# Kernel tuning notes

Measured on AMD Instinct MI355X. Metric: run time of the kernel, lower is better.

## Reference

```python
import jax, jax.numpy as jnp
import numpy as np

DIM = 32
HID = 128          # edge-MLP hidden width
N = 8192           # total nodes
E = 131072         # total edges
B = 64             # number of graphs
NUM_MP = 3
S2S_STEPS = 3


def setup_inputs() -> dict:
    key = jax.random.key(0)
    ks = jax.random.split(key, 24)
    g = lambda k, shape, s=0.05: jax.random.normal(k, shape, dtype=jnp.float32) * s

    inp = {
        "x": jax.random.normal(ks[0], (N, 1), dtype=jnp.float32),
        "edge_attr": jax.random.uniform(ks[1], (E, 2), dtype=jnp.float32),
        # params
        "lin0_w": g(ks[2], (1, DIM)), "lin0_b": g(ks[3], (DIM,)),
        "enn_w1": g(ks[4], (2, HID)), "enn_b1": g(ks[5], (HID,)),
        "enn_w2": g(ks[6], (HID, DIM * DIM)), "enn_b2": g(ks[7], (DIM * DIM,)),
        "root_w": g(ks[8], (DIM, DIM)), "conv_b": g(ks[9], (DIM,)),
        # GRU (gates ordered r,z,n as in torch)
        "gru_wih": g(ks[10], (DIM, 3 * DIM)), "gru_whh": g(ks[11], (DIM, 3 * DIM)),
        "gru_bih": g(ks[12], (3 * DIM,)), "gru_bhh": g(ks[13], (3 * DIM,)),
        # Set2Set LSTM: input 2*DIM, hidden DIM (gates ordered i,f,g,o as in torch)
        "s2s_wih": g(ks[14], (2 * DIM, 4 * DIM)), "s2s_whh": g(ks[15], (DIM, 4 * DIM)),
        "s2s_bih": g(ks[16], (4 * DIM,)), "s2s_bhh": g(ks[17], (4 * DIM,)),
        "lin1_w": g(ks[18], (2 * DIM, DIM)), "lin1_b": g(ks[19], (DIM,)),
        "lin2_w": g(ks[20], (DIM, 1)), "lin2_b": g(ks[21], (1,)),
        # int args
        "edge_index": jax.random.randint(ks[22], (2, E), 0, N, dtype=jnp.int32),
        "batch": jnp.sort(jax.random.randint(ks[23], (N,), 0, B, dtype=jnp.int32)),
    }
    return inp


def _forward(x, edge_attr, lin0_w, lin0_b, enn_w1, enn_b1, enn_w2, enn_b2,
             root_w, conv_b, gru_wih, gru_whh, gru_bih, gru_bhh,
             s2s_wih, s2s_whh, s2s_bih, s2s_bhh, lin1_w, lin1_b, lin2_w, lin2_b,
             edge_index, batch):
    src, dst = edge_index[0], edge_index[1]

    out = jax.nn.relu(x @ lin0_w + lin0_b)          # [N, DIM]
    h = out                                          # GRU hidden state

    # edge-conditioned weights (constant across MP layers -> hoisted)
    ew = jax.nn.relu(edge_attr @ enn_w1 + enn_b1) @ enn_w2 + enn_b2
    W = ew.reshape(E, DIM, DIM)                      # [E, in, out]

    deg = jnp.maximum(jax.ops.segment_sum(jnp.ones((E,), jnp.float32), dst,
                                          num_segments=N), 1.0)[:, None]

    for _ in range(NUM_MP):
        # NNConv: gather -> per-edge small matmul -> scatter-mean, + root + bias
        msg = jnp.einsum('ed,edo->eo', out[src], W)  # [E, DIM]
        agg = jax.ops.segment_sum(msg, dst, num_segments=N) / deg
        m = jax.nn.relu(agg + out @ root_w + conv_b)
        # GRU cell (single step)
        gi = m @ gru_wih + gru_bih
        gh = h @ gru_whh + gru_bhh
        ir, iz, in_ = jnp.split(gi, 3, axis=-1)
        hr, hz, hn = jnp.split(gh, 3, axis=-1)
        r = jax.nn.sigmoid(ir + hr)
        z = jax.nn.sigmoid(iz + hz)
        n = jnp.tanh(in_ + r * hn)
        h = (1.0 - z) * n + z * h
        out = h

    # Set2Set pooling
    qh = jnp.zeros((B, DIM), jnp.float32)
    qc = jnp.zeros((B, DIM), jnp.float32)
    q_star = jnp.zeros((B, 2 * DIM), jnp.float32)
    for _ in range(S2S_STEPS):
        gates = q_star @ s2s_wih + s2s_bih + qh @ s2s_whh + s2s_bhh
        i_, f_, g_, o_ = jnp.split(gates, 4, axis=-1)
        qc = jax.nn.sigmoid(f_) * qc + jax.nn.sigmoid(i_) * jnp.tanh(g_)
        qh = jax.nn.sigmoid(o_) * jnp.tanh(qc)       # [B, DIM]
        e = jnp.sum(out * qh[batch], axis=-1)        # [N] attention logits
        emax = jax.ops.segment_max(e, batch, num_segments=B)
        a = jnp.exp(e - emax[batch])
        a = a / jax.ops.segment_sum(a, batch, num_segments=B)[batch]
        r_read = jax.ops.segment_sum(a[:, None] * out, batch, num_segments=B)
        q_star = jnp.concatenate([qh, r_read], axis=-1)  # [B, 2*DIM]

    y = jax.nn.relu(q_star @ lin1_w + lin1_b) @ lin2_w + lin2_b
    return y.reshape(-1)                              # [B]


def reference(x, edge_attr, lin0_w, lin0_b, enn_w1, enn_b1, enn_w2, enn_b2,
              root_w, conv_b, gru_wih, gru_whh, gru_bih, gru_bhh,
              s2s_wih, s2s_whh, s2s_bih, s2s_bhh, lin1_w, lin1_b, lin2_w, lin2_b,
              edge_index, batch):
    return _forward(x, edge_attr, lin0_w, lin0_b, enn_w1, enn_b1, enn_w2, enn_b2,
                    root_w, conv_b, gru_wih, gru_whh, gru_bih, gru_bhh,
                    s2s_wih, s2s_whh, s2s_bih, s2s_bhh, lin1_w, lin1_b, lin2_w,
                    lin2_b, edge_index, batch)
```

## Files before the change

### kernel.cpp

```cpp
#include <hip/hip_runtime.h>

#define N_NODES 8192
#define N_EDGES 131072
#define NGRAPH  64
#define DIM     32
#define HID     128
#define KHALF   64
#define G_NODES 4
#define SROW    36
#define HROW    68
#define OROW    36
#define CEDGE   64
#define S2S_CAP 384

__device__ __forceinline__ float sigmoidf_(float x) { return 1.0f / (1.0f + expf(-x)); }

__global__ void prep1_kernel(const float* __restrict__ x, const float* __restrict__ w,
                             const float* __restrict__ b, float* __restrict__ out,
                             const int* __restrict__ dst, int* __restrict__ counts) {
  const int bb = blockIdx.x;
  if (bb < 1024) {
    int idx = bb * 256 + threadIdx.x;
    int n = idx >> 5, d = idx & 31;
    out[idx] = fmaxf(fmaf(x[n], w[d], b[d]), 0.0f);
  } else {
    int e = (bb - 1024) * 256 + threadIdx.x;
    atomicAdd(&counts[dst[e]], 1);
  }
}

__global__ void scan_kernel(const int* __restrict__ counts,
                            int* __restrict__ offsets,
                            float* __restrict__ deg_inv) {
  __shared__ int sm[1024];
  int t = threadIdx.x;
  int base = t * 8;
  int loc[8];
  int s = 0;
#pragma unroll
  for (int i = 0; i < 8; ++i) { loc[i] = s; s += counts[base + i]; }
  sm[t] = s;
  __syncthreads();
  for (int off = 1; off < 1024; off <<= 1) {
    int v = (t >= off) ? sm[t - off] : 0;
    __syncthreads();
    sm[t] += v;
    __syncthreads();
  }
  int excl = (t > 0) ? sm[t - 1] : 0;
#pragma unroll
  for (int i = 0; i < 8; ++i) {
    offsets[base + i] = excl + loc[i];
    int c = counts[base + i];
    deg_inv[base + i] = 1.0f / (float)(c > 0 ? c : 1);
  }
  if (t == 1023) offsets[N_NODES] = sm[1023];
}

__global__ void prep2_kernel(const int* __restrict__ ei, const float* __restrict__ ea,
                             const int* __restrict__ offsets, int* __restrict__ cursor,
                             int* __restrict__ csr_src, float2* __restrict__ csr_ea,
                             const int* __restrict__ batch, int* __restrict__ gstart) {
  const int bb = blockIdx.x;
  if (bb < 512) {
    int e = bb * 256 + threadIdx.x;
    int d = ei[N_EDGES + e];
    int pos = atomicAdd(&cursor[d], 1);
    int slot = offsets[d] + pos;
    csr_src[slot] = ei[e];
    csr_ea[slot] = make_float2(ea[2 * e], ea[2 * e + 1]);
  } else {
    int n = (bb - 512) * 256 + threadIdx.x;
    int b = batch[n];
    if (n == 0) {
      for (int g = 0; g <= b; ++g) gstart[g] = 0;
    } else {
      int bp = batch[n - 1];
      for (int g = bp + 1; g <= b; ++g) gstart[g] = n;
    }
    if (n == N_NODES - 1) {
      for (int g = b + 1; g <= NGRAPH; ++g) gstart[g] = N_NODES;
    }
  }
}

__global__ __launch_bounds__(256, 4) void mp_kernel(
    const float* __restrict__ out_cur, float* __restrict__ out_nxt,
    const int* __restrict__ offsets, const float* __restrict__ deg_inv,
    const int* __restrict__ csr_src, const float2* __restrict__ csr_ea,
    const float* __restrict__ w1, const float* __restrict__ b1,
    const float* __restrict__ w2, const float* __restrict__ b2,
    const float* __restrict__ root_w, const float* __restrict__ conv_b,
    const float* __restrict__ gwih, const float* __restrict__ gwhh,
    const float* __restrict__ gbih, const float* __restrict__ gbhh) {
  __shared__ float smem[G_NODES * KHALF * SROW];
  __shared__ float w1s[3 * HID];
  __shared__ float ebuf[G_NODES * DIM];
  __shared__ float mbuf[G_NODES * DIM];
  __shared__ float obuf[G_NODES * DIM];
  __shared__ int offs[G_NODES + 1];
  float* hidb = smem;
  float* osrcb = smem + CEDGE * HROW;
  float* S = smem;
  float* red = smem;

  const int t = threadIdx.x;
  const int node0 = blockIdx.x * G_NODES;

  if (t <= G_NODES) offs[t] = offsets[node0 + t];
  if (t < HID) {
    w1s[t] = w1[t];
    w1s[HID + t] = w1[HID + t];
    w1s[2 * HID + t] = b1[t];
  }

  const int kg = t >> 4, dg = t & 15;
  const int k0 = kg * 4, d0 = dg * 2;
  const int ec = t >> 2, sub = t & 3;
  const int ks = t >> 4;
  const int dvh = (t >> 3) & 1;
  const int og = t & 7;

  float a4[G_NODES][4];
#pragma unroll
  for (int g = 0; g < G_NODES; ++g)
#pragma unroll
    for (int r = 0; r < 4; ++r) a4[g][r] = 0.0f;
  float oacc[G_NODES] = {0.0f, 0.0f, 0.0f, 0.0f};
  __syncthreads();

  const int ebase = offs[0], eend = offs[G_NODES];

  for (int half = 0; half < 2; ++half) {
    float acc[G_NODES][4][2];
#pragma unroll
    for (int g = 0; g < G_NODES; ++g)
#pragma unroll
      for (int i = 0; i < 4; ++i) { acc[g][i][0] = 0.0f; acc[g][i][1] = 0.0f; }

    for (int c0 = ebase; c0 < eend; c0 += CEDGE) {
      const int cnt = min(CEDGE, eend - c0);
      if (ec < cnt) {
        const int slot = c0 + ec;
        const float2 eav = csr_ea[slot];
        const int sidx = csr_src[slot];
#pragma unroll
        for (int q = 0; q < 4; ++q) {
          const int kl = sub * 16 + q * 4;
          const int kgl = half * KHALF + kl;
          const float4 wx = *(const float4*)(w1s + kgl);
          const float4 wy = *(const float4*)(w1s + HID + kgl);
          const float4 bv = *(const float4*)(w1s + 2 * HID + kgl);
          float4 hv;
          hv.x = fmaxf(fmaf(eav.y, wy.x, fmaf(eav.x, wx.x, bv.x)), 0.0f);
          hv.y = fmaxf(fmaf(eav.y, wy.y, fmaf(eav.x, wx.y, bv.y)), 0.0f);
          hv.z = fmaxf(fmaf(eav.y, wy.z, fmaf(eav.x, wx.z, bv.z)), 0.0f);
          hv.w = fmaxf(fmaf(eav.y, wy.w, fmaf(eav.x, wx.w, bv.w)), 0.0f);
          *(float4*)(hidb + ec * HROW + kl) = hv;
        }
        *(float4*)(osrcb + ec * OROW + sub * 8) =
            *(const float4*)(out_cur + sidx * DIM + sub * 8);
        *(float4*)(osrcb + ec * OROW + sub * 8 + 4) =
            *(const float4*)(out_cur + sidx * DIM + sub * 8 + 4);
      }
      __syncthreads();
#pragma unroll
      for (int g = 0; g < G_NODES; ++g) {
        const int es = max(offs[g], c0) - c0;
        const int ee = min(offs[g + 1], c0 + cnt) - c0;
        for (int e = es; e < ee; ++e) {
          const float4 hv = *(const float4*)(hidb + e * HROW + k0);
          const float2 ov = *(const float2*)(osrcb + e * OROW + d0);
          acc[g][0][0] = fmaf(hv.x, ov.x, acc[g][0][0]);
          acc[g][0][1] = fmaf(hv.x, ov.y, acc[g][0][1]);
          acc[g][1][0] = fmaf(hv.y, ov.x, acc[g][1][0]);
          acc[g][1][1] = fmaf(hv.y, ov.y, acc[g][1][1]);
          acc[g][2][0] = fmaf(hv.z, ov.x, acc[g][2][0]);
          acc[g][2][1] = fmaf(hv.z, ov.y, acc[g][2][1]);
          acc[g][3][0] = fmaf(hv.w, ov.x, acc[g][3][0]);
          acc[g][3][1] = fmaf(hv.w, ov.y, acc[g][3][1]);
          if (half == 0 && t < DIM) oacc[g] += osrcb[e * OROW + t];
        }
      }
      __syncthreads();
    }

    {
      const int dd = (d0 + (kg & 3) * 8) & 31;
#pragma unroll
      for (int g = 0; g < G_NODES; ++g) {
        float* Sg = S + g * KHALF * SROW;
#pragma unroll
        for (int i = 0; i < 4; ++i)
          *(float2*)(Sg + (k0 + i) * SROW + dd) =
              make_float2(acc[g][i][0], acc[g][i][1]);
      }
    }
    __syncthreads();

    {
      const int shift = (ks & 3) * 8;
#pragma unroll
      for (int i = 0; i < 4; ++i) {
        const int kl = ks * 4 + i;
        const float* w2k = w2 + (size_t)(half * KHALF + kl) * (DIM * DIM);
#pragma unroll
        for (int q = 0; q < 4; ++q) {
          const int dbase = dvh * 16 + q * 4;
          const int dq = (dbase + shift) & 31;
          float4 sv[G_NODES];
#pragma unroll
          for (int g = 0; g < G_NODES; ++g)
            sv[g] = *(const float4*)(S + (g * KHALF + kl) * SROW + dq);
#pragma unroll
          for (int r = 0; r < 4; ++r) {
            const float4 wv = *(const float4*)(w2k + (dbase + r) * DIM + og * 4);
#pragma unroll
            for (int g = 0; g < G_NODES; ++g) {
              const float s = ((const float*)&sv[g])[r];
              a4[g][0] = fmaf(s, wv.x, a4[g][0]);
              a4[g][1] = fmaf(s, wv.y, a4[g][1]);
              a4[g][2] = fmaf(s, wv.z, a4[g][2]);
              a4[g][3] = fmaf(s, wv.w, a4[g][3]);
            }
          }
        }
      }
    }
    __syncthreads();
  }

#pragma unroll
  for (int g = 0; g < G_NODES; ++g)
#pragma unroll
    for (int r = 0; r < 4; ++r) red[(g * 4 + r) * 257 + t] = a4[g][r];
  if (t < DIM) {
#pragma unroll
    for (int g = 0; g < G_NODES; ++g) obuf[g * DIM + t] = oacc[g];
  }
  if (t < G_NODES * DIM) ebuf[t] = out_cur[node0 * DIM + t];
  __syncthreads();

  if (t < G_NODES * DIM) {
    const int g = t >> 5, o = t & 31;
    const int node = node0 + g;
    const float* rp = red + (g * 4 + (o & 3)) * 257 + (o >> 2);
    float sum = 0.0f;
#pragma unroll
    for (int j = 0; j < 32; ++j) sum += rp[j * 8];
    float ob2 = 0.0f;
#pragma unroll
    for (int d = 0; d < DIM; ++d) ob2 = fmaf(obuf[g * DIM + d], b2[d * DIM + o], ob2);
    const float agg = (sum + ob2) * deg_inv[node];
    float rt = conv_b[o];
#pragma unroll
    for (int d = 0; d < DIM; ++d) rt = fmaf(ebuf[g * DIM + d], root_w[d * DIM + o], rt);
    mbuf[t] = fmaxf(agg + rt, 0.0f);
  }
  __syncthreads();
  if (t < G_NODES * DIM) {
    const int g = t >> 5, o = t & 31;
    const int node = node0 + g;
    float gi[3], gh[3];
#pragma unroll
    for (int jj = 0; jj < 3; ++jj) {
      float si = gbih[jj * DIM + o], sh = gbhh[jj * DIM + o];
#pragma unroll
      for (int d = 0; d < DIM; ++d) {
        si = fmaf(mbuf[g * DIM + d], gwih[d * 3 * DIM + jj * DIM + o], si);
        sh = fmaf(ebuf[g * DIM + d], gwhh[d * 3 * DIM + jj * DIM + o], sh);
      }
      gi[jj] = si;
      gh[jj] = sh;
    }
    const float r = sigmoidf_(gi[0] + gh[0]);
    const float z = sigmoidf_(gi[1] + gh[1]);
    const float nn = tanhf(fmaf(r, gh[2], gi[2]));
    out_nxt[node * DIM + o] = (1.0f - z) * nn + z * ebuf[t];
  }
}

__global__ __launch_bounds__(256) void s2s_kernel(
    const float* __restrict__ outf, const int* __restrict__ gstart,
    const float* __restrict__ wih, const float* __restrict__ whh,
    const float* __restrict__ bih, const float* __restrict__ bhh,
    const float* __restrict__ l1w, const float* __restrict__ l1b,
    const float* __restrict__ l2w, const float* __restrict__ l2b,
    float* __restrict__ y) {
  __shared__ float rows[S2S_CAP * DIM];
  __shared__ float qh[DIM], qc[DIM], qstar[2 * DIM], gates[4 * DIM];
  __shared__ float wsum[4], wmax[4], wr[4][DIM];
  const int b = blockIdx.x, t = threadIdx.x;
  const int gs = gstart[b], ge = gstart[b + 1];
  const int cnt = ge - gs;
  const int w = t >> 6, lane = t & 63;
  const bool use_lds = (cnt <= S2S_CAP);
  if (use_lds) {
    for (int j = t * 4; j < cnt * DIM; j += 1024)
      *(float4*)(rows + j) = *(const float4*)(outf + (size_t)gs * DIM + j);
  }
  const float* R = use_lds ? (const float*)rows : outf + (size_t)gs * DIM;
  if (t < DIM) { qh[t] = 0.0f; qc[t] = 0.0f; }
  if (t < 2 * DIM) qstar[t] = 0.0f;
  __syncthreads();
  for (int step = 0; step < 3; ++step) {
    if (t < 4 * DIM) {
      float gv = bih[t] + bhh[t];
      for (int i = 0; i < 2 * DIM; ++i) gv = fmaf(qstar[i], wih[i * 4 * DIM + t], gv);
      for (int i = 0; i < DIM; ++i) gv = fmaf(qh[i], whh[i * 4 * DIM + t], gv);
      gates[t] = gv;
    }
    __syncthreads();
    if (t < DIM) {
      const float ig = sigmoidf_(gates[t]);
      const float fg = sigmoidf_(gates[DIM + t]);
      const float gg = tanhf(gates[2 * DIM + t]);
      const float og = sigmoidf_(gates[3 * DIM + t]);
      const float c = fmaf(fg, qc[t], ig * gg);
      qc[t] = c;
      qh[t] = og * tanhf(c);
    }
    __syncthreads();
    float lmax = -INFINITY;
    for (int n = t; n < cnt; n += 256) {
      const float* orow = R + n * DIM;
      float e = 0.0f;
#pragma unroll
      for (int d = 0; d < DIM; ++d) e = fmaf(orow[d], qh[d], e);
      lmax = fmaxf(lmax, e);
    }
#pragma unroll
    for (int off = 32; off > 0; off >>= 1) lmax = fmaxf(lmax, __shfl_xor(lmax, off));
    if (lane == 0) wmax[w] = lmax;
    __syncthreads();
    const float gmax = fmaxf(fmaxf(wmax[0], wmax[1]), fmaxf(wmax[2], wmax[3]));
    float rl[DIM];
#pragma unroll
    for (int d = 0; d < DIM; ++d) rl[d] = 0.0f;
    float lsum = 0.0f;
    for (int n = t; n < cnt; n += 256) {
      const float* orow = R + n * DIM;
      float e = 0.0f;
#pragma unroll
      for (int d = 0; d < DIM; ++d) e = fmaf(orow[d], qh[d], e);
      const float a = expf(e - gmax);
      lsum += a;
#pragma unroll
      for (int d = 0; d < DIM; ++d) rl[d] = fmaf(a, orow[d], rl[d]);
    }
#pragma unroll
    for (int off = 32; off > 0; off >>= 1) {
      lsum += __shfl_xor(lsum, off);
#pragma unroll
      for (int d = 0; d < DIM; ++d) rl[d] += __shfl_xor(rl[d], off);
    }
    __syncthreads();
    if (lane == 0) {
      wsum[w] = lsum;
#pragma unroll
      for (int d = 0; d < DIM; ++d) wr[w][d] = rl[d];
    }
    __syncthreads();
    if (t < DIM) {
      const float stot = wsum[0] + wsum[1] + wsum[2] + wsum[3];
      const float rv = wr[0][t] + wr[1][t] + wr[2][t] + wr[3][t];
      qstar[t] = qh[t];
      qstar[DIM + t] = (stot > 0.0f) ? rv / stot : 0.0f;
    }
    __syncthreads();
  }
  if (t < DIM) {
    float u = l1b[t];
    for (int i = 0; i < 2 * DIM; ++i) u = fmaf(qstar[i], l1w[i * DIM + t], u);
    u = fmaxf(u, 0.0f);
    float v = u * l2w[t];
#pragma unroll
    for (int off = 16; off > 0; off >>= 1) v += __shfl_xor(v, off);
    if (t == 0) y[b] = v + l2b[0];
  }
}

extern "C" void kernel_launch(void* const* d_in, const int* in_sizes, int n_in,
                              void* d_out, int out_size, void* d_ws, size_t ws_size,
                              hipStream_t stream) {
  const float* x        = (const float*)d_in[0];
  const float* ea       = (const float*)d_in[1];
  const float* lin0_w   = (const float*)d_in[2];
  const float* lin0_b   = (const float*)d_in[3];
  const float* enn_w1   = (const float*)d_in[4];
  const float* enn_b1   = (const float*)d_in[5];
  const float* enn_w2   = (const float*)d_in[6];
  const float* enn_b2   = (const float*)d_in[7];
  const float* root_w   = (const float*)d_in[8];
  const float* conv_b   = (const float*)d_in[9];
  const float* gru_wih  = (const float*)d_in[10];
  const float* gru_whh  = (const float*)d_in[11];
  const float* gru_bih  = (const float*)d_in[12];
  const float* gru_bhh  = (const float*)d_in[13];
  const float* s2s_wih  = (const float*)d_in[14];
  const float* s2s_whh  = (const float*)d_in[15];
  const float* s2s_bih  = (const float*)d_in[16];
  const float* s2s_bhh  = (const float*)d_in[17];
  const float* lin1_w   = (const float*)d_in[18];
  const float* lin1_b   = (const float*)d_in[19];
  const float* lin2_w   = (const float*)d_in[20];
  const float* lin2_b   = (const float*)d_in[21];
  const int*   ei       = (const int*)d_in[22];
  const int*   batch    = (const int*)d_in[23];
  float* y = (float*)d_out;

  char* p = (char*)d_ws;
  auto alloc = [&](size_t bytes) -> void* {
    void* r = (void*)p;
    p += (bytes + 255) & ~(size_t)255;
    return r;
  };
  float*  out_a   = (float*)alloc(N_NODES * DIM * 4);
  float*  out_b   = (float*)alloc(N_NODES * DIM * 4);
  int*    counts  = (int*)alloc(N_NODES * 4);
  int*    cursor  = (int*)alloc(N_NODES * 4);
  int*    offsets = (int*)alloc((N_NODES + 1) * 4);
  int*    csr_src = (int*)alloc(N_EDGES * 4);
  float2* csr_ea  = (float2*)alloc(N_EDGES * 8);
  float*  deg_inv = (float*)alloc(N_NODES * 4);
  int*    gstart  = (int*)alloc((NGRAPH + 1) * 4);
  (void)ws_size; (void)n_in; (void)in_sizes; (void)out_size;

  hipMemsetAsync(counts, 0, (size_t)2 * N_NODES * 4, stream);

  prep1_kernel<<<1024 + 512, 256, 0, stream>>>(x, lin0_w, lin0_b, out_a,
                                               ei + N_EDGES, counts);
  scan_kernel<<<1, 1024, 0, stream>>>(counts, offsets, deg_inv);
  prep2_kernel<<<512 + 32, 256, 0, stream>>>(ei, ea, offsets, cursor, csr_src,
                                             csr_ea, batch, gstart);

  const int ngroups = N_NODES / G_NODES;
  const float* cur = out_a;
  float* nxt = out_b;
  for (int layer = 0; layer < 3; ++layer) {
    mp_kernel<<<ngroups, 256, 0, stream>>>(
        cur, nxt, offsets, deg_inv, csr_src, csr_ea, enn_w1, enn_b1, enn_w2,
        enn_b2, root_w, conv_b, gru_wih, gru_whh, gru_bih, gru_bhh);
    const float* tmp = cur; cur = nxt; nxt = (float*)tmp;
  }

  s2s_kernel<<<NGRAPH, 256, 0, stream>>>(cur, gstart, s2s_wih, s2s_whh, s2s_bih,
                                         s2s_bhh, lin1_w, lin1_b, lin2_w, lin2_b, y);
}
```

Measured before the change: 435.0 us.

## Process full 128-wide hidden dimension in one pass instead of two halves

The message-passing kernel used to split the 128-wide edge-MLP hidden dimension into two halves, walking the edge list and recomputing the hidden activations and gathering source features twice. It now handles all 128 hidden units in one edge pass, with each thread holding 4x4 accumulators per node, and stores the full S tile in dynamic LDS (about 73 KB) before one w2 contraction. This removes the duplicated edge gathers, the extra passes and the barriers between them. The cost is much higher LDS and register use per block, with launch bounds lowered to 2 blocks, so occupancy drops.

Measured after the change: 1.014 ms. 2.33x slower.

```diff
diff --git a/kernel.cpp b/kernel.cpp
--- a/kernel.cpp
+++ b/kernel.cpp
@@ -5,13 +5,13 @@
 #define NGRAPH  64
 #define DIM     32
 #define HID     128
-#define KHALF   64
 #define G_NODES 4
 #define SROW    36
-#define HROW    68
+#define HROW    132
 #define OROW    36
 #define CEDGE   64
 #define S2S_CAP 384
+#define DYN_LDS (G_NODES * HID * SROW * 4)
 
 __device__ __forceinline__ float sigmoidf_(float x) { return 1.0f / (1.0f + expf(-x)); }
 
@@ -84,7 +84,7 @@
   }
 }
 
-__global__ __launch_bounds__(256, 4) void mp_kernel(
+__global__ __launch_bounds__(256, 2) void mp_kernel(
     const float* __restrict__ out_cur, float* __restrict__ out_nxt,
     const int* __restrict__ offsets, const float* __restrict__ deg_inv,
     const int* __restrict__ csr_src, const float2* __restrict__ csr_ea,
@@ -93,7 +93,7 @@
     const float* __restrict__ root_w, const float* __restrict__ conv_b,
     const float* __restrict__ gwih, const float* __restrict__ gwhh,
     const float* __restrict__ gbih, const float* __restrict__ gbhh) {
-  __shared__ float smem[G_NODES * KHALF * SROW];
+  extern __shared__ float smem[];
   __shared__ float w1s[3 * HID];
   __shared__ float ebuf[G_NODES * DIM];
   __shared__ float mbuf[G_NODES * DIM];
@@ -114,131 +114,128 @@
     w1s[2 * HID + t] = b1[t];
   }
 
-  const int kg = t >> 4, dg = t & 15;
-  const int k0 = kg * 4, d0 = dg * 2;
+  const int kg = t >> 3, dg = t & 7;
+  const int k0 = kg * 4, d0 = dg * 4;
   const int ec = t >> 2, sub = t & 3;
-  const int ks = t >> 4;
-  const int dvh = (t >> 3) & 1;
-  const int og = t & 7;
+
+  float acc[G_NODES][4][4];
+#pragma unroll
+  for (int g = 0; g < G_NODES; ++g)
+#pragma unroll
+    for (int i = 0; i < 4; ++i)
+#pragma unroll
+      for (int j = 0; j < 4; ++j) acc[g][i][j] = 0.0f;
+  float oacc[G_NODES] = {0.0f, 0.0f, 0.0f, 0.0f};
+  __syncthreads();
+
+  const int ebase = offs[0], eend = offs[G_NODES];
+  for (int c0 = ebase; c0 < eend; c0 += CEDGE) {
+    const int cnt = min(CEDGE, eend - c0);
+    if (ec < cnt) {
+      const int slot = c0 + ec;
+      const float2 eav = csr_ea[slot];
+      const int sidx = csr_src[slot];
+#pragma unroll
+      for (int q = 0; q < 8; ++q) {
+        const int k4 = sub * 32 + q * 4;
+        const float4 wx = *(const float4*)(w1s + k4);
+        const float4 wy = *(const float4*)(w1s + HID + k4);
+        const float4 bv = *(const float4*)(w1s + 2 * HID + k4);
+        float4 hv;
+        hv.x = fmaxf(fmaf(eav.y, wy.x, fmaf(eav.x, wx.x, bv.x)), 0.0f);
+        hv.y = fmaxf(fmaf(eav.y, wy.y, fmaf(eav.x, wx.y, bv.y)), 0.0f);
+        hv.z = fmaxf(fmaf(eav.y, wy.z, fmaf(eav.x, wx.z, bv.z)), 0.0f);
+        hv.w = fmaxf(fmaf(eav.y, wy.w, fmaf(eav.x, wx.w, bv.w)), 0.0f);
+        *(float4*)(hidb + ec * HROW + k4) = hv;
+      }
+      *(float4*)(osrcb + ec * OROW + sub * 8) =
+          *(const float4*)(out_cur + sidx * DIM + sub * 8);
+      *(float4*)(osrcb + ec * OROW + sub * 8 + 4) =
+          *(const float4*)(out_cur + sidx * DIM + sub * 8 + 4);
+    }
+    __syncthreads();
+#pragma unroll
+    for (int g = 0; g < G_NODES; ++g) {
+      const int es = max(offs[g], c0) - c0;
+      const int ee = min(offs[g + 1], c0 + cnt) - c0;
+      for (int e = es; e < ee; ++e) {
+        const float4 hv = *(const float4*)(hidb + e * HROW + k0);
+        const float4 ov = *(const float4*)(osrcb + e * OROW + d0);
+        acc[g][0][0] = fmaf(hv.x, ov.x, acc[g][0][0]);
+        acc[g][0][1] = fmaf(hv.x, ov.y, acc[g][0][1]);
+        acc[g][0][2] = fmaf(hv.x, ov.z, acc[g][0][2]);
+        acc[g][0][3] = fmaf(hv.x, ov.w, acc[g][0][3]);
+        acc[g][1][0] = fmaf(hv.y, ov.x, acc[g][1][0]);
+        acc[g][1][1] = fmaf(hv.y, ov.y, acc[g][1][1]);
+        acc[g][1][2] = fmaf(hv.y, ov.z, acc[g][1][2]);
+        acc[g][1][3] = fmaf(hv.y, ov.w, acc[g][1][3]);
+        acc[g][2][0] = fmaf(hv.z, ov.x, acc[g][2][0]);
+        acc[g][2][1] = fmaf(hv.z, ov.y, acc[g][2][1]);
+        acc[g][2][2] = fmaf(hv.z, ov.z, acc[g][2][2]);
+        acc[g][2][3] = fmaf(hv.z, ov.w, acc[g][2][3]);
+        acc[g][3][0] = fmaf(hv.w, ov.x, acc[g][3][0]);
+        acc[g][3][1] = fmaf(hv.w, ov.y, acc[g][3][1]);
+        acc[g][3][2] = fmaf(hv.w, ov.z, acc[g][3][2]);
+        acc[g][3][3] = fmaf(hv.w, ov.w, acc[g][3][3]);
+        if (t < DIM) oacc[g] += osrcb[e * OROW + t];
+      }
+    }
+    __syncthreads();
+  }
+
+#pragma unroll
+  for (int g = 0; g < G_NODES; ++g) {
+#pragma unroll
+    for (int i = 0; i < 4; ++i)
+      *(float4*)(S + (g * HID + k0 + i) * SROW + d0) =
+          make_float4(acc[g][i][0], acc[g][i][1], acc[g][i][2], acc[g][i][3]);
+  }
+  if (t < DIM) {
+#pragma unroll
+    for (int g = 0; g < G_NODES; ++g) obuf[g * DIM + t] = oacc[g];
+  }
+  if (t < G_NODES * DIM) ebuf[t] = out_cur[node0 * DIM + t];
+  __syncthreads();
 
   float a4[G_NODES][4];
 #pragma unroll
   for (int g = 0; g < G_NODES; ++g)
 #pragma unroll
     for (int r = 0; r < 4; ++r) a4[g][r] = 0.0f;
-  float oacc[G_NODES] = {0.0f, 0.0f, 0.0f, 0.0f};
-  __syncthreads();
-
-  const int ebase = offs[0], eend = offs[G_NODES];
-
-  for (int half = 0; half < 2; ++half) {
-    float acc[G_NODES][4][2];
-#pragma unroll
-    for (int g = 0; g < G_NODES; ++g)
-#pragma unroll
-      for (int i = 0; i < 4; ++i) { acc[g][i][0] = 0.0f; acc[g][i][1] = 0.0f; }
-
-    for (int c0 = ebase; c0 < eend; c0 += CEDGE) {
-      const int cnt = min(CEDGE, eend - c0);
-      if (ec < cnt) {
-        const int slot = c0 + ec;
-        const float2 eav = csr_ea[slot];
-        const int sidx = csr_src[slot];
-#pragma unroll
-        for (int q = 0; q < 4; ++q) {
-          const int kl = sub * 16 + q * 4;
-          const int kgl = half * KHALF + kl;
-          const float4 wx = *(const float4*)(w1s + kgl);
-          const float4 wy = *(const float4*)(w1s + HID + kgl);
-          const float4 bv = *(const float4*)(w1s + 2 * HID + kgl);
-          float4 hv;
-          hv.x = fmaxf(fmaf(eav.y, wy.x, fmaf(eav.x, wx.x, bv.x)), 0.0f);
-          hv.y = fmaxf(fmaf(eav.y, wy.y, fmaf(eav.x, wx.y, bv.y)), 0.0f);
-          hv.z = fmaxf(fmaf(eav.y, wy.z, fmaf(eav.x, wx.z, bv.z)), 0.0f);
-          hv.w = fmaxf(fmaf(eav.y, wy.w, fmaf(eav.x, wx.w, bv.w)), 0.0f);
-          *(float4*)(hidb + ec * HROW + kl) = hv;
-        }
-        *(float4*)(osrcb + ec * OROW + sub * 8) =
-            *(const float4*)(out_cur + sidx * DIM + sub * 8);
-        *(float4*)(osrcb + ec * OROW + sub * 8 + 4) =
-            *(const float4*)(out_cur + sidx * DIM + sub * 8 + 4);
-      }
-      __syncthreads();
-#pragma unroll
-      for (int g = 0; g < G_NODES; ++g) {
-        const int es = max(offs[g], c0) - c0;
-        const int ee = min(offs[g + 1], c0 + cnt) - c0;
-        for (int e = es; e < ee; ++e) {
-          const float4 hv = *(const float4*)(hidb + e * HROW + k0);
-          const float2 ov = *(const float2*)(osrcb + e * OROW + d0);
-          acc[g][0][0] = fmaf(hv.x, ov.x, acc[g][0][0]);
-          acc[g][0][1] = fmaf(hv.x, ov.y, acc[g][0][1]);
-          acc[g][1][0] = fmaf(hv.y, ov.x, acc[g][1][0]);
-          acc[g][1][1] = fmaf(hv.y, ov.y, acc[g][1][1]);
-          acc[g][2][0] = fmaf(hv.z, ov.x, acc[g][2][0]);
-          acc[g][2][1] = fmaf(hv.z, ov.y, acc[g][2][1]);
-          acc[g][3][0] = fmaf(hv.w, ov.x, acc[g][3][0]);
-          acc[g][3][1] = fmaf(hv.w, ov.y, acc[g][3][1]);
-          if (half == 0 && t < DIM) oacc[g] += osrcb[e * OROW + t];
-        }
-      }
-      __syncthreads();
-    }
-
-    {
-      const int dd = (d0 + (kg & 3) * 8) & 31;
-#pragma unroll
-      for (int g = 0; g < G_NODES; ++g) {
-        float* Sg = S + g * KHALF * SROW;
-#pragma unroll
-        for (int i = 0; i < 4; ++i)
-          *(float2*)(Sg + (k0 + i) * SROW + dd) =
-              make_float2(acc[g][i][0], acc[g][i][1]);
-      }
-    }
-    __syncthreads();
-
-    {
-      const int shift = (ks & 3) * 8;
-#pragma unroll
-      for (int i = 0; i < 4; ++i) {
-        const int kl = ks * 4 + i;
-        const float* w2k = w2 + (size_t)(half * KHALF + kl) * (DIM * DIM);
-#pragma unroll
-        for (int q = 0; q < 4; ++q) {
-          const int dbase = dvh * 16 + q * 4;
-          const int dq = (dbase + shift) & 31;
-          float4 sv[G_NODES];
-#pragma unroll
-          for (int g = 0; g < G_NODES; ++g)
-            sv[g] = *(const float4*)(S + (g * KHALF + kl) * SROW + dq);
-#pragma unroll
-          for (int r = 0; r < 4; ++r) {
-            const float4 wv = *(const float4*)(w2k + (dbase + r) * DIM + og * 4);
-#pragma unroll
-            for (int g = 0; g < G_NODES; ++g) {
-              const float s = ((const float*)&sv[g])[r];
-              a4[g][0] = fmaf(s, wv.x, a4[g][0]);
-              a4[g][1] = fmaf(s, wv.y, a4[g][1]);
-              a4[g][2] = fmaf(s, wv.z, a4[g][2]);
-              a4[g][3] = fmaf(s, wv.w, a4[g][3]);
-            }
+  {
+    const int ks = t >> 3;
+    const int og = t & 7;
+#pragma unroll
+    for (int i = 0; i < 4; ++i) {
+      const int kl = ks * 4 + i;
+      const float* w2k = w2 + (size_t)kl * (DIM * DIM);
+#pragma unroll
+      for (int q = 0; q < 8; ++q) {
+        const int dq = ((q + ks) & 7) * 4;
+        float4 sv[G_NODES];
+#pragma unroll
+        for (int g = 0; g < G_NODES; ++g)
+          sv[g] = *(const float4*)(S + (g * HID + kl) * SROW + dq);
+#pragma unroll
+        for (int r = 0; r < 4; ++r) {
+          const float4 wv = *(const float4*)(w2k + (dq + r) * DIM + og * 4);
+#pragma unroll
+          for (int g = 0; g < G_NODES; ++g) {
+            const float s = ((const float*)&sv[g])[r];
+            a4[g][0] = fmaf(s, wv.x, a4[g][0]);
+            a4[g][1] = fmaf(s, wv.y, a4[g][1]);
+            a4[g][2] = fmaf(s, wv.z, a4[g][2]);
+            a4[g][3] = fmaf(s, wv.w, a4[g][3]);
           }
         }
       }
     }
-    __syncthreads();
-  }
-
+  }
+  __syncthreads();
 #pragma unroll
   for (int g = 0; g < G_NODES; ++g)
 #pragma unroll
     for (int r = 0; r < 4; ++r) red[(g * 4 + r) * 257 + t] = a4[g][r];
-  if (t < DIM) {
-#pragma unroll
-    for (int g = 0; g < G_NODES; ++g) obuf[g * DIM + t] = oacc[g];
-  }
-  if (t < G_NODES * DIM) ebuf[t] = out_cur[node0 * DIM + t];
   __syncthreads();
 
   if (t < G_NODES * DIM) {
@@ -409,6 +406,11 @@
   const int*   batch    = (const int*)d_in[23];
   float* y = (float*)d_out;
 
+  static int lds_set = 0;
+  (void)lds_set;
+  hipFuncSetAttribute((const void*)mp_kernel,
+                      hipFuncAttributeMaxDynamicSharedMemorySize, DYN_LDS);
+
   char* p = (char*)d_ws;
   auto alloc = [&](size_t bytes) -> void* {
     void* r = (void*)p;
@@ -438,7 +440,7 @@
   const float* cur = out_a;
   float* nxt = out_b;
   for (int layer = 0; layer < 3; ++layer) {
-    mp_kernel<<<ngroups, 256, 0, stream>>>(
+    mp_kernel<<<ngroups, 256, DYN_LDS, stream>>>(
         cur, nxt, offsets, deg_inv, csr_src, csr_ea, enn_w1, enn_b1, enn_w2,
         enn_b2, root_w, conv_b, gru_wih, gru_whh, gru_bih, gru_bhh);
     const float* tmp = cur; cur = nxt; nxt = (float*)tmp;
```

## Restructure message-passing kernel: 8 nodes per block, per-wave edge loops, K in four passes

Applied to the files above, without the earlier changes.

The message-passing kernel now handles 8 nodes per block instead of 4. Each wave walks the edges of two nodes directly from global memory, prefetching the next edge's source features into registers, instead of staging 64-edge chunks of hidden activations and source rows in LDS behind block barriers. The hidden dimension is split into four passes of 32, and each pass's W2 contraction now serves 8 nodes, doubling reuse of every W2 load. The cost is more registers (a 64-entry accumulator per thread), load imbalance across waves when node degrees differ, and half as many blocks.

Result: slower. 1.650 ms (+279.4%).

```diff
diff --git a/kernel.cpp b/kernel.cpp
--- a/kernel.cpp
+++ b/kernel.cpp
@@ -5,12 +5,10 @@
 #define NGRAPH  64
 #define DIM     32
 #define HID     128
-#define KHALF   64
-#define G_NODES 4
+#define G_NODES 8
+#define P_K     32
 #define SROW    36
-#define HROW    68
-#define OROW    36
-#define CEDGE   64
+#define RPAD    65
 #define S2S_CAP 384
 
 __device__ __forceinline__ float sigmoidf_(float x) { return 1.0f / (1.0f + expf(-x)); }
@@ -93,135 +91,129 @@
     const float* __restrict__ root_w, const float* __restrict__ conv_b,
     const float* __restrict__ gwih, const float* __restrict__ gwhh,
     const float* __restrict__ gbih, const float* __restrict__ gbhh) {
-  __shared__ float smem[G_NODES * KHALF * SROW];
-  __shared__ float w1s[3 * HID];
+  __shared__ float S[G_NODES * P_K * SROW];
   __shared__ float ebuf[G_NODES * DIM];
-  __shared__ float mbuf[G_NODES * DIM];
+  __shared__ float mbuf[128];
   __shared__ float obuf[G_NODES * DIM];
   __shared__ int offs[G_NODES + 1];
-  float* hidb = smem;
-  float* osrcb = smem + CEDGE * HROW;
-  float* S = smem;
-  float* red = smem;
+  float* red = S;
 
   const int t = threadIdx.x;
   const int node0 = blockIdx.x * G_NODES;
+  const int w = t >> 6, lane = t & 63;
+  const int kg = lane >> 2, dg = lane & 3;
+  const int ks = t >> 4, dq = (t >> 2) & 3, oq = t & 3;
 
   if (t <= G_NODES) offs[t] = offsets[node0 + t];
-  if (t < HID) {
-    w1s[t] = w1[t];
-    w1s[HID + t] = w1[HID + t];
-    w1s[2 * HID + t] = b1[t];
-  }
-
-  const int kg = t >> 4, dg = t & 15;
-  const int k0 = kg * 4, d0 = dg * 2;
-  const int ec = t >> 2, sub = t & 3;
-  const int ks = t >> 4;
-  const int dvh = (t >> 3) & 1;
-  const int og = t & 7;
-
-  float a4[G_NODES][4];
+
+  float a4[G_NODES][8];
 #pragma unroll
   for (int g = 0; g < G_NODES; ++g)
 #pragma unroll
-    for (int r = 0; r < 4; ++r) a4[g][r] = 0.0f;
-  float oacc[G_NODES] = {0.0f, 0.0f, 0.0f, 0.0f};
+    for (int o = 0; o < 8; ++o) a4[g][o] = 0.0f;
   __syncthreads();
 
-  const int ebase = offs[0], eend = offs[G_NODES];
-
-  for (int half = 0; half < 2; ++half) {
-    float acc[G_NODES][4][2];
-#pragma unroll
-    for (int g = 0; g < G_NODES; ++g)
-#pragma unroll
-      for (int i = 0; i < 4; ++i) { acc[g][i][0] = 0.0f; acc[g][i][1] = 0.0f; }
-
-    for (int c0 = ebase; c0 < eend; c0 += CEDGE) {
-      const int cnt = min(CEDGE, eend - c0);
-      if (ec < cnt) {
-        const int slot = c0 + ec;
-        const float2 eav = csr_ea[slot];
-        const int sidx = csr_src[slot];
-#pragma unroll
-        for (int q = 0; q < 4; ++q) {
-          const int kl = sub * 16 + q * 4;
-          const int kgl = half * KHALF + kl;
-          const float4 wx = *(const float4*)(w1s + kgl);
-          const float4 wy = *(const float4*)(w1s + HID + kgl);
-          const float4 bv = *(const float4*)(w1s + 2 * HID + kgl);
-          float4 hv;
-          hv.x = fmaxf(fmaf(eav.y, wy.x, fmaf(eav.x, wx.x, bv.x)), 0.0f);
-          hv.y = fmaxf(fmaf(eav.y, wy.y, fmaf(eav.x, wx.y, bv.y)), 0.0f);
-          hv.z = fmaxf(fmaf(eav.y, wy.z, fmaf(eav.x, wx.z, bv.z)), 0.0f);
-          hv.w = fmaxf(fmaf(eav.y, wy.w, fmaf(eav.x, wx.w, bv.w)), 0.0f);
-          *(float4*)(hidb + ec * HROW + kl) = hv;
+  for (int pass = 0; pass < 4; ++pass) {
+    const int klg0 = pass * P_K + kg * 2;
+    const float2 w1x = *(const float2*)(w1 + klg0);
+    const float2 w1y = *(const float2*)(w1 + HID + klg0);
+    const float2 b1v = *(const float2*)(b1 + klg0);
+#pragma unroll
+    for (int s = 0; s < 2; ++s) {
+      const int g = w * 2 + s;
+      const int eb = offs[g], ee = offs[g + 1];
+      float acc0[8], acc1[8], oacc[8];
+#pragma unroll
+      for (int j = 0; j < 8; ++j) { acc0[j] = 0.0f; acc1[j] = 0.0f; oacc[j] = 0.0f; }
+      float2 ea_n = make_float2(0.0f, 0.0f);
+      float4 ovn0 = make_float4(0, 0, 0, 0), ovn1 = make_float4(0, 0, 0, 0);
+      if (eb < ee) {
+        const int sn = csr_src[eb];
+        ea_n = csr_ea[eb];
+        ovn0 = *(const float4*)(out_cur + sn * DIM + dg * 8);
+        ovn1 = *(const float4*)(out_cur + sn * DIM + dg * 8 + 4);
+      }
+      for (int e = eb; e < ee; ++e) {
+        const float2 eav = ea_n;
+        const float4 ov0 = ovn0, ov1 = ovn1;
+        if (e + 1 < ee) {
+          const int sn = csr_src[e + 1];
+          ea_n = csr_ea[e + 1];
+          ovn0 = *(const float4*)(out_cur + sn * DIM + dg * 8);
+          ovn1 = *(const float4*)(out_cur + sn * DIM + dg * 8 + 4);
         }
-        *(float4*)(osrcb + ec * OROW + sub * 8) =
-            *(const float4*)(out_cur + sidx * DIM + sub * 8);
-        *(float4*)(osrcb + ec * OROW + sub * 8 + 4) =
-            *(const float4*)(out_cur + sidx * DIM + sub * 8 + 4);
-      }
-      __syncthreads();
-#pragma unroll
-      for (int g = 0; g < G_NODES; ++g) {
-        const int es = max(offs[g], c0) - c0;
-        const int ee = min(offs[g + 1], c0 + cnt) - c0;
-        for (int e = es; e < ee; ++e) {
-          const float4 hv = *(const float4*)(hidb + e * HROW + k0);
-          const float2 ov = *(const float2*)(osrcb + e * OROW + d0);
-          acc[g][0][0] = fmaf(hv.x, ov.x, acc[g][0][0]);
-          acc[g][0][1] = fmaf(hv.x, ov.y, acc[g][0][1]);
-          acc[g][1][0] = fmaf(hv.y, ov.x, acc[g][1][0]);
-          acc[g][1][1] = fmaf(hv.y, ov.y, acc[g][1][1]);
-          acc[g][2][0] = fmaf(hv.z, ov.x, acc[g][2][0]);
-          acc[g][2][1] = fmaf(hv.z, ov.y, acc[g][2][1]);
-          acc[g][3][0] = fmaf(hv.w, ov.x, acc[g][3][0]);
-          acc[g][3][1] = fmaf(hv.w, ov.y, acc[g][3][1]);
-          if (half == 0 && t < DIM) oacc[g] += osrcb[e * OROW + t];
+        const float h0 =
+            fmaxf(fmaf(eav.y, w1y.x, fmaf(eav.x, w1x.x, b1v.x)), 0.0f);
+        const float h1 =
+            fmaxf(fmaf(eav.y, w1y.y, fmaf(eav.x, w1x.y, b1v.y)), 0.0f);
+        acc0[0] = fmaf(h0, ov0.x, acc0[0]);
+        acc0[1] = fmaf(h0, ov0.y, acc0[1]);
+        acc0[2] = fmaf(h0, ov0.z, acc0[2]);
+        acc0[3] = fmaf(h0, ov0.w, acc0[3]);
+        acc0[4] = fmaf(h0, ov1.x, acc0[4]);
+        acc0[5] = fmaf(h0, ov1.y, acc0[5]);
+        acc0[6] = fmaf(h0, ov1.z, acc0[6]);
+        acc0[7] = fmaf(h0, ov1.w, acc0[7]);
+        acc1[0] = fmaf(h1, ov0.x, acc1[0]);
+        acc1[1] = fmaf(h1, ov0.y, acc1[1]);
+        acc1[2] = fmaf(h1, ov0.z, acc1[2]);
+        acc1[3] = fmaf(h1, ov0.w, acc1[3]);
+        acc1[4] = fmaf(h1, ov1.x, acc1[4]);
+        acc1[5] = fmaf(h1, ov1.y, acc1[5]);
+        acc1[6] = fmaf(h1, ov1.z, acc1[6]);
+        acc1[7] = fmaf(h1, ov1.w, acc1[7]);
+        if (pass == 0) {
+          oacc[0] += ov0.x; oacc[1] += ov0.y; oacc[2] += ov0.z; oacc[3] += ov0.w;
+          oacc[4] += ov1.x; oacc[5] += ov1.y; oacc[6] += ov1.z; oacc[7] += ov1.w;
         }
       }
-      __syncthreads();
-    }
+      const int rot = (kg & 7) * 4;
+      const int p0 = (dg * 8 + rot) & 31;
+      const int p1 = (dg * 8 + 4 + rot) & 31;
+      float* Sg = S + (g * P_K + kg * 2) * SROW;
+      *(float4*)(Sg + p0) = make_float4(acc0[0], acc0[1], acc0[2], acc0[3]);
+      *(float4*)(Sg + p1) = make_float4(acc0[4], acc0[5], acc0[6], acc0[7]);
+      *(float4*)(Sg + SROW + p0) = make_float4(acc1[0], acc1[1], acc1[2], acc1[3]);
+      *(float4*)(Sg + SROW + p1) = make_float4(acc1[4], acc1[5], acc1[6], acc1[7]);
+      if (pass == 0 && kg == 0) {
+        *(float4*)(obuf + g * DIM + dg * 8) =
+            make_float4(oacc[0], oacc[1], oacc[2], oacc[3]);
+        *(float4*)(obuf + g * DIM + dg * 8 + 4) =
+            make_float4(oacc[4], oacc[5], oacc[6], oacc[7]);
+      }
+    }
+    __syncthreads();
 
     {
-      const int dd = (d0 + (kg & 3) * 8) & 31;
-#pragma unroll
-      for (int g = 0; g < G_NODES; ++g) {
-        float* Sg = S + g * KHALF * SROW;
-#pragma unroll
-        for (int i = 0; i < 4; ++i)
-          *(float2*)(Sg + (k0 + i) * SROW + dd) =
-              make_float2(acc[g][i][0], acc[g][i][1]);
-      }
-    }
-    __syncthreads();
-
-    {
-      const int shift = (ks & 3) * 8;
-#pragma unroll
-      for (int i = 0; i < 4; ++i) {
-        const int kl = ks * 4 + i;
-        const float* w2k = w2 + (size_t)(half * KHALF + kl) * (DIM * DIM);
-#pragma unroll
-        for (int q = 0; q < 4; ++q) {
-          const int dbase = dvh * 16 + q * 4;
-          const int dq = (dbase + shift) & 31;
+      const int rot = (ks & 7) * 4;
+#pragma unroll
+      for (int i = 0; i < 2; ++i) {
+        const int kl = ks * 2 + i;
+        const float* w2k = w2 + (size_t)(pass * P_K + kl) * (DIM * DIM);
+#pragma unroll
+        for (int dd = 0; dd < 2; ++dd) {
+          const int dbase = dq * 8 + dd * 4;
+          const int pos = (dbase + rot) & 31;
           float4 sv[G_NODES];
 #pragma unroll
           for (int g = 0; g < G_NODES; ++g)
-            sv[g] = *(const float4*)(S + (g * KHALF + kl) * SROW + dq);
+            sv[g] = *(const float4*)(S + (g * P_K + kl) * SROW + pos);
 #pragma unroll
           for (int r = 0; r < 4; ++r) {
-            const float4 wv = *(const float4*)(w2k + (dbase + r) * DIM + og * 4);
+            const float* w2d = w2k + (dbase + r) * DIM + oq * 8;
+            const float4 wv0 = *(const float4*)(w2d);
+            const float4 wv1 = *(const float4*)(w2d + 4);
 #pragma unroll
             for (int g = 0; g < G_NODES; ++g) {
-              const float s = ((const float*)&sv[g])[r];
-              a4[g][0] = fmaf(s, wv.x, a4[g][0]);
-              a4[g][1] = fmaf(s, wv.y, a4[g][1]);
-              a4[g][2] = fmaf(s, wv.z, a4[g][2]);
-              a4[g][3] = fmaf(s, wv.w, a4[g][3]);
+              const float sg = ((const float*)&sv[g])[r];
+              a4[g][0] = fmaf(sg, wv0.x, a4[g][0]);
+              a4[g][1] = fmaf(sg, wv0.y, a4[g][1]);
+              a4[g][2] = fmaf(sg, wv0.z, a4[g][2]);
+              a4[g][3] = fmaf(sg, wv0.w, a4[g][3]);
+              a4[g][4] = fmaf(sg, wv1.x, a4[g][4]);
+              a4[g][5] = fmaf(sg, wv1.y, a4[g][5]);
+              a4[g][6] = fmaf(sg, wv1.z, a4[g][6]);
+              a4[g][7] = fmaf(sg, wv1.w, a4[g][7]);
             }
           }
         }
@@ -230,53 +222,57 @@
     __syncthreads();
   }
 
-#pragma unroll
-  for (int g = 0; g < G_NODES; ++g)
-#pragma unroll
-    for (int r = 0; r < 4; ++r) red[(g * 4 + r) * 257 + t] = a4[g][r];
-  if (t < DIM) {
-#pragma unroll
-    for (int g = 0; g < G_NODES; ++g) obuf[g * DIM + t] = oacc[g];
-  }
-  if (t < G_NODES * DIM) ebuf[t] = out_cur[node0 * DIM + t];
-  __syncthreads();
-
-  if (t < G_NODES * DIM) {
-    const int g = t >> 5, o = t & 31;
-    const int node = node0 + g;
-    const float* rp = red + (g * 4 + (o & 3)) * 257 + (o >> 2);
-    float sum = 0.0f;
-#pragma unroll
-    for (int j = 0; j < 32; ++j) sum += rp[j * 8];
-    float ob2 = 0.0f;
-#pragma unroll
-    for (int d = 0; d < DIM; ++d) ob2 = fmaf(obuf[g * DIM + d], b2[d * DIM + o], ob2);
-    const float agg = (sum + ob2) * deg_inv[node];
-    float rt = conv_b[o];
-#pragma unroll
-    for (int d = 0; d < DIM; ++d) rt = fmaf(ebuf[g * DIM + d], root_w[d * DIM + o], rt);
-    mbuf[t] = fmaxf(agg + rt, 0.0f);
-  }
-  __syncthreads();
-  if (t < G_NODES * DIM) {
-    const int g = t >> 5, o = t & 31;
-    const int node = node0 + g;
-    float gi[3], gh[3];
-#pragma unroll
-    for (int jj = 0; jj < 3; ++jj) {
-      float si = gbih[jj * DIM + o], sh = gbhh[jj * DIM + o];
-#pragma unroll
-      for (int d = 0; d < DIM; ++d) {
-        si = fmaf(mbuf[g * DIM + d], gwih[d * 3 * DIM + jj * DIM + o], si);
-        sh = fmaf(ebuf[g * DIM + d], gwhh[d * 3 * DIM + jj * DIM + o], sh);
+  ebuf[t] = out_cur[node0 * DIM + t];
+
+  for (int gb = 0; gb < 2; ++gb) {
+    __syncthreads();
+    const int contrib = ks * 4 + dq;
+#pragma unroll
+    for (int g2 = 0; g2 < 4; ++g2)
+#pragma unroll
+      for (int oo = 0; oo < 8; ++oo)
+        red[(g2 * 32 + oq * 8 + oo) * RPAD + contrib] = a4[gb * 4 + g2][oo];
+    __syncthreads();
+    if (t < 128) {
+      const int g2 = t >> 5, o = t & 31;
+      const int g = gb * 4 + g2;
+      const int node = node0 + g;
+      const float* rp = red + (g2 * 32 + o) * RPAD;
+      float sum = 0.0f;
+#pragma unroll
+      for (int j = 0; j < 64; ++j) sum += rp[j];
+      float ob2 = 0.0f;
+#pragma unroll
+      for (int d = 0; d < DIM; ++d) ob2 = fmaf(obuf[g * DIM + d], b2[d * DIM + o], ob2);
+      const float agg = (sum + ob2) * deg_inv[node];
+      float rt = conv_b[o];
+#pragma unroll
+      for (int d = 0; d < DIM; ++d)
+        rt = fmaf(ebuf[g * DIM + d], root_w[d * DIM + o], rt);
+      mbuf[t] = fmaxf(agg + rt, 0.0f);
+    }
+    __syncthreads();
+    if (t < 128) {
+      const int g2 = t >> 5, o = t & 31;
+      const int g = gb * 4 + g2;
+      const int node = node0 + g;
+      float gi[3], gh[3];
+#pragma unroll
+      for (int jj = 0; jj < 3; ++jj) {
+        float si = gbih[jj * DIM + o], sh = gbhh[jj * DIM + o];
+#pragma unroll
+        for (int d = 0; d < DIM; ++d) {
+          si = fmaf(mbuf[g2 * DIM + d], gwih[d * 3 * DIM + jj * DIM + o], si);
+          sh = fmaf(ebuf[g * DIM + d], gwhh[d * 3 * DIM + jj * DIM + o], sh);
+        }
+        gi[jj] = si;
+        gh[jj] = sh;
       }
-      gi[jj] = si;
-      gh[jj] = sh;
-    }
-    const float r = sigmoidf_(gi[0] + gh[0]);
-    const float z = sigmoidf_(gi[1] + gh[1]);
-    const float nn = tanhf(fmaf(r, gh[2], gi[2]));
-    out_nxt[node * DIM + o] = (1.0f - z) * nn + z * ebuf[t];
+      const float r = sigmoidf_(gi[0] + gh[0]);
+      const float z = sigmoidf_(gi[1] + gh[1]);
+      const float nn = tanhf(fmaf(r, gh[2], gi[2]));
+      out_nxt[node * DIM + o] = (1.0f - z) * nn + z * ebuf[g * DIM + o];
+    }
   }
 }
 
@@ -434,11 +430,11 @@
   prep2_kernel<<<512 + 32, 256, 0, stream>>>(ei, ea, offsets, cursor, csr_src,
                                              csr_ea, batch, gstart);
 
-  const int ngroups = N_NODES / G_NODES;
+  const int nblocks = N_NODES / G_NODES;
   const float* cur = out_a;
   float* nxt = out_b;
   for (int layer = 0; layer < 3; ++layer) {
-    mp_kernel<<<ngroups, 256, 0, stream>>>(
+    mp_kernel<<<nblocks, 256, 0, stream>>>(
         cur, nxt, offsets, deg_inv, csr_src, csr_ea, enn_w1, enn_b1, enn_w2,
         enn_b2, root_w, conv_b, gru_wih, gru_whh, gru_bih, gru_bhh);
     const float* tmp = cur; cur = nxt; nxt = (float*)tmp;
```
